# Kernel tuning notes

Measured on AMD Instinct MI355X. Metric: run time of the kernel, lower is better.

The kernel has to match this reference:

```python
import jax, jax.numpy as jnp
import numpy as np

B, T, D = 4, 2048, 2048
H, DK, DV = 16, 128, 128


def setup_inputs() -> dict:
    key = jax.random.key(0)
    ks = jax.random.split(key, 8)
    s = 1.0 / np.sqrt(D)
    return {
        "q": jax.random.normal(ks[0], (B, T, D), jnp.float32),
        "k": jax.random.normal(ks[1], (B, T, D), jnp.float32),
        "v": jax.random.normal(ks[2], (B, T, D), jnp.float32),
        "mask": jnp.tril(jnp.ones((T, T), dtype=bool)),  # True = attend
        # weights stored as [in, out] (torch Linear applies x @ W.T)
        "Wq": jax.random.normal(ks[3], (D, H * DK), jnp.float32) * s,
        "Wk": jax.random.normal(ks[4], (D, H * DK), jnp.float32) * s,
        "Wv": jax.random.normal(ks[5], (D, H * DV), jnp.float32) * s,
        "Wo": jax.random.normal(ks[6], (H * DV, D), jnp.float32) * s,
    }


def _attention(q, k, v, mask, Wq, Wk, Wv, Wo):
    # project and split heads: [B,T,H*dh] -> [B,H,T,dh]
    def split_heads(x, dh):
        b, t, _ = x.shape
        return x.reshape(b, t, H, dh).transpose(0, 2, 1, 3)

    q_i = split_heads(q @ Wq, DK)
    k_i = split_heads(k @ Wk, DK)
    v_i = split_heads(v @ Wv, DV)

    scores = jnp.einsum("bhik,bhjk->bhij", q_i, k_i) / jnp.sqrt(
        jnp.asarray(DK, q_i.dtype)
    )
    neg = -jnp.finfo(scores.dtype).max
    scores = jnp.where(mask[None, None, :, :], scores, neg)
    attn = jax.nn.softmax(scores, axis=-1)
    vals = jnp.einsum("bhij,bhjv->bhiv", attn, v_i)  # [B,H,T,dv]
    merged = vals.transpose(0, 2, 1, 3).reshape(q.shape[0], q.shape[1], H * DV)
    return merged @ Wo


def reference(q, k, v, mask, Wq, Wk, Wv, Wo):
    return _attention(q, k, v, mask, Wq, Wk, Wv, Wo)
```

## Files before the change

kernel.cpp:

```cpp
#include <hip/hip_runtime.h>
#include <hip/hip_bf16.h>

typedef __attribute__((ext_vector_type(8))) short bf16x8;
typedef __attribute__((ext_vector_type(4))) unsigned short u16x4;
typedef __attribute__((ext_vector_type(4))) float f32x4;

constexpr int Bb = 4, Tt = 2048, Dd = 2048, Hh = 16, DHd = 128;

static __device__ __forceinline__ unsigned short f2bf(float f) {
  union { float f; unsigned u; } x; x.f = f;
  unsigned r = x.u + 0x7fffu + ((x.u >> 16) & 1u);
  return (unsigned short)(r >> 16);
}

static __device__ __forceinline__ void gld16(const void* g, void* l) {
  __builtin_amdgcn_global_load_lds(
      (__attribute__((address_space(1))) void*)g,
      (__attribute__((address_space(3))) void*)l, 16, 0, 0);
}

__global__ __launch_bounds__(256) void cvt_bf16(const float* __restrict__ s,
                                                unsigned short* __restrict__ d) {
  const size_t i = ((size_t)blockIdx.x * 256 + threadIdx.x) * 8;
  float4 a = *(const float4*)(s + i);
  float4 b = *(const float4*)(s + i + 4);
  bf16x8 pk;
  pk[0] = (short)f2bf(a.x); pk[1] = (short)f2bf(a.y);
  pk[2] = (short)f2bf(a.z); pk[3] = (short)f2bf(a.w);
  pk[4] = (short)f2bf(b.x); pk[5] = (short)f2bf(b.y);
  pk[6] = (short)f2bf(b.z); pk[7] = (short)f2bf(b.w);
  *(bf16x8*)(d + i) = pk;
}

__global__ __launch_bounds__(256) void wtrans_all(
    const float* __restrict__ Wq, const float* __restrict__ Wk,
    const float* __restrict__ Wv, const float* __restrict__ Wo,
    unsigned short* __restrict__ WqT, unsigned short* __restrict__ WkT,
    unsigned short* __restrict__ WvT, unsigned short* __restrict__ WoT,
    float qscale) {
  __shared__ __align__(16) unsigned short tile[64][72];
  const float* src;
  unsigned short* dst;
  float sc = 1.0f;
  switch (blockIdx.z) {
    case 0: src = Wq; dst = WqT; sc = qscale; break;
    case 1: src = Wk; dst = WkT; break;
    case 2: src = Wv; dst = WvT; break;
    default: src = Wo; dst = WoT; break;
  }
  const int t = threadIdx.x;
  const int k0 = blockIdx.x * 64, n0 = blockIdx.y * 64;
  const int c = t & 15, r = t >> 4;
#pragma unroll
  for (int p = 0; p < 4; ++p) {
    const int rr = r + 16 * p;
    float4 v = *(const float4*)(src + (size_t)(k0 + rr) * Dd + n0 + c * 4);
    u16x4 pk;
    pk[0] = f2bf(v.x * sc); pk[1] = f2bf(v.y * sc);
    pk[2] = f2bf(v.z * sc); pk[3] = f2bf(v.w * sc);
    *(u16x4*)&tile[rr][c * 4] = pk;
  }
  __syncthreads();
#pragma unroll
  for (int p = 0; p < 4; ++p) {
    const int nn = r + 16 * p;
    u16x4 pk;
    pk[0] = tile[c * 4 + 0][nn]; pk[1] = tile[c * 4 + 1][nn];
    pk[2] = tile[c * 4 + 2][nn]; pk[3] = tile[c * 4 + 3][nn];
    *(u16x4*)(dst + (size_t)(n0 + nn) * Dd + k0 + c * 4) = pk;
  }
}

template <int OMODE>
__global__ __launch_bounds__(512, 2) void gemm256(
    const unsigned short* __restrict__ A, const unsigned short* __restrict__ Bt,
    void* __restrict__ Outp) {
  __shared__ __align__(16) unsigned short As[4 * 8192];
  __shared__ __align__(16) unsigned short Bs[4 * 8192];
  const int t = threadIdx.x, lane = t & 63, w = t >> 6;
  const int wm = w >> 2, wn = w & 3;
  const int fr = lane & 15, fq = lane >> 4;
  const int slot = blockIdx.x;
  const int orig = (slot & 7) * 32 + (slot >> 3);
  const int m0 = (orig >> 3) * 256, n0 = (orig & 7) * 256;

  f32x4 acc[8][4] = {};
  const int aoff = (wm * 128 + fr) * 32 + fq * 8;
  const int boff = (wn * 64 + fr) * 32 + fq * 8;

  auto STAGE = [&](int kt) {
    const int b = kt & 3;
    const int k0 = kt * 32;
#pragma unroll
    for (int p = 0; p < 2; ++p) {
      const int idx = t + p * 512, row = idx >> 2, ch = idx & 3;
      gld16(A + (size_t)(m0 + row) * Dd + k0 + ch * 8, &As[b * 8192 + idx * 8]);
    }
#pragma unroll
    for (int p = 0; p < 2; ++p) {
      const int idx = t + p * 512, row = idx >> 2, ch = idx & 3;
      gld16(Bt + (size_t)(n0 + row) * Dd + k0 + ch * 8, &Bs[b * 8192 + idx * 8]);
    }
  };

  constexpr int NT = Dd / 32;
  STAGE(0); STAGE(1); STAGE(2);

  for (int kt = 0; kt < NT; ++kt) {
    if (kt + 3 < NT) {
      STAGE(kt + 3);
      asm volatile("s_waitcnt vmcnt(12)" ::: "memory");
    } else if (kt + 2 < NT) {
      asm volatile("s_waitcnt vmcnt(8)" ::: "memory");
    } else if (kt + 1 < NT) {
      asm volatile("s_waitcnt vmcnt(4)" ::: "memory");
    } else {
      asm volatile("s_waitcnt vmcnt(0)" ::: "memory");
    }
    __builtin_amdgcn_sched_barrier(0);
    __builtin_amdgcn_s_barrier();
    __builtin_amdgcn_sched_barrier(0);

    const int bo = (kt & 3) * 8192;
    bf16x8 af[8], bf[4];
#pragma unroll
    for (int m = 0; m < 8; ++m)
      af[m] = *(const bf16x8*)&As[bo + aoff + m * 512];
#pragma unroll
    for (int n = 0; n < 4; ++n)
      bf[n] = *(const bf16x8*)&Bs[bo + boff + n * 512];

    __builtin_amdgcn_s_setprio(1);
#pragma unroll
    for (int m = 0; m < 8; ++m)
#pragma unroll
      for (int n = 0; n < 4; ++n)
        acc[m][n] = __builtin_amdgcn_mfma_f32_16x16x32_bf16(af[m], bf[n],
                                                            acc[m][n], 0, 0, 0);
    __builtin_amdgcn_s_setprio(0);
    __builtin_amdgcn_sched_barrier(0);
    __builtin_amdgcn_s_barrier();
  }

#pragma unroll
  for (int m = 0; m < 8; ++m) {
    const int mg = m0 + wm * 128 + m * 16 + fq * 4;
    const int bb = mg >> 11, tt0 = mg & (Tt - 1);
#pragma unroll
    for (int n = 0; n < 4; ++n) {
      const int ng = n0 + wn * 64 + n * 16 + fr;
      if (OMODE == 0) {
        float* o = (float*)Outp + (size_t)mg * Dd + ng;
#pragma unroll
        for (int r = 0; r < 4; ++r) o[(size_t)r * Dd] = acc[m][n][r];
      } else if (OMODE == 1) {
        const int h = ng >> 7, dh = ng & 127;
        unsigned short* o = (unsigned short*)Outp +
                            (((size_t)bb * Hh + h) * Tt + tt0) * DHd + dh;
#pragma unroll
        for (int r = 0; r < 4; ++r) o[r * DHd] = f2bf(acc[m][n][r]);
      } else {
        const int h = ng >> 7, dh = ng & 127;
        u16x4 pk;
#pragma unroll
        for (int r = 0; r < 4; ++r) pk[r] = f2bf(acc[m][n][r]);
        *(u16x4*)((unsigned short*)Outp +
                  (((size_t)bb * Hh + h) * DHd + dh) * Tt + tt0) = pk;
      }
    }
  }
}

__global__ __launch_bounds__(256, 2) void fattn(
    const unsigned short* __restrict__ Qp, const unsigned short* __restrict__ Kp,
    const unsigned short* __restrict__ Vt, unsigned short* __restrict__ Ao) {
  __shared__ __align__(16) unsigned short Ks[2][64 * 128];
  __shared__ __align__(16) unsigned short Vs[2][128 * 64];
  const int t = threadIdx.x, lane = t & 63, w = t >> 6;
  const int fr = lane & 15, fq = lane >> 4;
  const int rsw = fr & 7;
  const int id = blockIdx.x;
  const int xcd = id & 7, slot = id >> 3;
  const int bh = xcd * 8 + (slot >> 4);
  const int qb = 15 - (slot & 15);
  const int q0w = qb * 128 + w * 32;
  const unsigned short* Qb = Qp + (size_t)bh * Tt * DHd;
  const unsigned short* Kb = Kp + (size_t)bh * Tt * DHd;
  const unsigned short* Vb = Vt + (size_t)bh * DHd * Tt;

  bf16x8 qf[2][4];
#pragma unroll
  for (int mg = 0; mg < 2; ++mg)
#pragma unroll
    for (int ks = 0; ks < 4; ++ks)
      qf[mg][ks] = *(const bf16x8*)(Qb + (size_t)(q0w + mg * 16 + fr) * DHd +
                                    ks * 32 + fq * 8);

  f32x4 oacc[2][8] = {};
  float m_[2] = {-1e30f, -1e30f};
  float l_[2] = {0.f, 0.f};

  auto STAGE = [&](int b, int kv0) {
#pragma unroll
    for (int p = 0; p < 4; ++p) {
      const int idx = t + p * 256, row = idx >> 4, ch = idx & 15;
      gld16(Kb + (size_t)(kv0 + row) * DHd + ((ch ^ (row & 7)) * 8),
            &Ks[b][idx * 8]);
    }
#pragma unroll
    for (int p = 0; p < 4; ++p) {
      const int idx = t + p * 256, row = idx >> 3, ch = idx & 7;
      gld16(Vb + (size_t)row * Tt + kv0 + ((ch ^ (row & 7)) * 8),
            &Vs[b][idx * 8]);
    }
  };

  const int ntile = 2 * qb + 2;
  STAGE(0, 0);
  int cur = 0;

  for (int kt = 0; kt < ntile; ++kt) {
    const int kv0 = kt * 64;
    __builtin_amdgcn_s_barrier();
    if (kt + 1 < ntile) {
      STAGE(cur ^ 1, (kt + 1) * 64);
      asm volatile("s_waitcnt vmcnt(8)" ::: "memory");
    } else {
      asm volatile("s_waitcnt vmcnt(0)" ::: "memory");
    }
    __builtin_amdgcn_sched_barrier(0);
    __builtin_amdgcn_s_barrier();

    if (kv0 <= q0w + 31) {
      const unsigned short* Kc = &Ks[cur][0];
      const unsigned short* Vc = &Vs[cur][0];

      f32x4 s[2][4] = {};
      __builtin_amdgcn_s_setprio(1);
#pragma unroll
      for (int tt = 0; tt < 4; ++tt) {
        bf16x8 kf[4];
#pragma unroll
        for (int ks = 0; ks < 4; ++ks)
          kf[ks] = *(const bf16x8*)(Kc + (tt * 16 + fr) * 128 +
                                    ((ks * 4 + fq) ^ rsw) * 8);
#pragma unroll
        for (int ks = 0; ks < 4; ++ks) {
          s[0][tt] = __builtin_amdgcn_mfma_f32_16x16x32_bf16(kf[ks], qf[0][ks],
                                                             s[0][tt], 0, 0, 0);
          s[1][tt] = __builtin_amdgcn_mfma_f32_16x16x32_bf16(kf[ks], qf[1][ks],
                                                             s[1][tt], 0, 0, 0);
        }
      }
      __builtin_amdgcn_s_setprio(0);

      uint2 c[2][4];
#pragma unroll
      for (int mg = 0; mg < 2; ++mg) {
        const int qg = q0w + mg * 16;
        if (kv0 + 63 > qg) {
          const int qa = qg + fr;
#pragma unroll
          for (int tt = 0; tt < 4; ++tt)
#pragma unroll
            for (int r = 0; r < 4; ++r)
              if (kv0 + tt * 16 + fq * 4 + r > qa) s[mg][tt][r] = -1e30f;
        }

        float tmax = s[mg][0][0];
#pragma unroll
        for (int tt = 0; tt < 4; ++tt)
#pragma unroll
          for (int r = 0; r < 4; ++r) tmax = fmaxf(tmax, s[mg][tt][r]);
        tmax = fmaxf(tmax, __shfl_xor(tmax, 16));
        tmax = fmaxf(tmax, __shfl_xor(tmax, 32));

        if (!__all(tmax <= m_[mg] + 8.0f)) {
          const float mn = fmaxf(m_[mg], tmax);
          const float alpha = __builtin_amdgcn_exp2f(m_[mg] - mn);
          m_[mg] = mn;
          float al4[4];
#pragma unroll
          for (int r = 0; r < 4; ++r) al4[r] = __shfl(alpha, fq * 4 + r);
#pragma unroll
          for (int dt = 0; dt < 8; ++dt)
#pragma unroll
            for (int r = 0; r < 4; ++r) oacc[mg][dt][r] *= al4[r];
          l_[mg] *= alpha;
        }

        float rs = 0.f;
#pragma unroll
        for (int tt = 0; tt < 4; ++tt)
#pragma unroll
          for (int r = 0; r < 4; ++r) {
            const float p = __builtin_amdgcn_exp2f(s[mg][tt][r] - m_[mg]);
            s[mg][tt][r] = p;
            rs += p;
          }
        rs += __shfl_xor(rs, 16);
        rs += __shfl_xor(rs, 32);
        l_[mg] += rs;

#pragma unroll
        for (int tt = 0; tt < 4; ++tt) {
          unsigned r0, r1;
          asm("v_cvt_pk_bf16_f32 %0, %1, %2"
              : "=v"(r0) : "v"(s[mg][tt][0]), "v"(s[mg][tt][1]));
          asm("v_cvt_pk_bf16_f32 %0, %1, %2"
              : "=v"(r1) : "v"(s[mg][tt][2]), "v"(s[mg][tt][3]));
          c[mg][tt].x = r0; c[mg][tt].y = r1;
        }
      }

      const int src0 = fr + 32 * (fq & 1);
      const int src1 = src0 + 16;
      const bool hi = (fq >> 1) != 0;
      __builtin_amdgcn_s_setprio(1);
#pragma unroll
      for (int ks2 = 0; ks2 < 2; ++ks2) {
        bf16x8 pf[2];
#pragma unroll
        for (int mg = 0; mg < 2; ++mg) {
          const int a0 = __shfl((int)c[mg][2 * ks2].x, src0);
          const int b0 = __shfl((int)c[mg][2 * ks2 + 1].x, src0);
          const int a1 = __shfl((int)c[mg][2 * ks2].y, src0);
          const int b1 = __shfl((int)c[mg][2 * ks2 + 1].y, src0);
          const int a2 = __shfl((int)c[mg][2 * ks2].x, src1);
          const int b2 = __shfl((int)c[mg][2 * ks2 + 1].x, src1);
          const int a3 = __shfl((int)c[mg][2 * ks2].y, src1);
          const int b3 = __shfl((int)c[mg][2 * ks2 + 1].y, src1);
          union { int wd[4]; bf16x8 v; } pu;
          pu.wd[0] = hi ? b0 : a0;
          pu.wd[1] = hi ? b1 : a1;
          pu.wd[2] = hi ? b2 : a2;
          pu.wd[3] = hi ? b3 : a3;
          pf[mg] = pu.v;
        }
#pragma unroll
        for (int dt = 0; dt < 8; ++dt) {
          const bf16x8 vf = *(const bf16x8*)(Vc + (dt * 16 + fr) * 64 +
                                             ((ks2 * 4 + fq) ^ rsw) * 8);
          oacc[0][dt] = __builtin_amdgcn_mfma_f32_16x16x32_bf16(pf[0], vf,
                                                                oacc[0][dt], 0, 0, 0);
          oacc[1][dt] = __builtin_amdgcn_mfma_f32_16x16x32_bf16(pf[1], vf,
                                                                oacc[1][dt], 0, 0, 0);
        }
      }
      __builtin_amdgcn_s_setprio(0);
    }
    cur ^= 1;
  }

  const int bb = bh >> 4, hh = bh & 15;
#pragma unroll
  for (int mg = 0; mg < 2; ++mg) {
    float linv[4];
#pragma unroll
    for (int r = 0; r < 4; ++r) linv[r] = 1.0f / __shfl(l_[mg], fq * 4 + r);
    const int qrow = q0w + mg * 16 + fq * 4;
#pragma unroll
    for (int r = 0; r < 4; ++r) {
      unsigned short* o = Ao + ((size_t)bb * Tt + qrow + r) * Dd + hh * DHd + fr;
#pragma unroll
      for (int dt = 0; dt < 8; ++dt) o[dt * 16] = f2bf(oacc[mg][dt][r] * linv[r]);
    }
  }
}

extern "C" void kernel_launch(void* const* d_in, const int* in_sizes, int n_in,
                              void* d_out, int out_size, void* d_ws, size_t ws_size,
                              hipStream_t stream) {
  const float* q = (const float*)d_in[0];
  const float* k = (const float*)d_in[1];
  const float* v = (const float*)d_in[2];
  const float* Wq = (const float*)d_in[4];
  const float* Wk = (const float*)d_in[5];
  const float* Wv = (const float*)d_in[6];
  const float* Wo = (const float*)d_in[7];

  const size_t WE = (size_t)Dd * Dd;
  const size_t PE = (size_t)Bb * Hh * Tt * DHd;
  unsigned short* WqT = (unsigned short*)d_ws;
  unsigned short* WkT = WqT + WE;
  unsigned short* WvT = WkT + WE;
  unsigned short* WoT = WvT + WE;
  unsigned short* Qx = WoT + WE;
  unsigned short* Kx = Qx + PE;
  unsigned short* Vx = Kx + PE;
  unsigned short* Ax = Vx + PE;

  const float qscale = (float)(1.4426950408889634 / 11.313708498984761);
  wtrans_all<<<dim3(32, 32, 4), 256, 0, stream>>>(
      Wq, Wk, Wv, Wo, WqT, WkT, WvT, WoT, qscale);

  cvt_bf16<<<dim3(8192), 256, 0, stream>>>(q, Ax);
  gemm256<1><<<dim3(256), 512, 0, stream>>>(Ax, WqT, Qx);
  cvt_bf16<<<dim3(8192), 256, 0, stream>>>(k, Ax);
  gemm256<1><<<dim3(256), 512, 0, stream>>>(Ax, WkT, Kx);
  cvt_bf16<<<dim3(8192), 256, 0, stream>>>(v, Ax);
  gemm256<2><<<dim3(256), 512, 0, stream>>>(Ax, WvT, Vx);
  fattn<<<dim3(1024), 256, 0, stream>>>(Qx, Kx, Vx, Ax);
  gemm256<0><<<dim3(256), 512, 0, stream>>>(Ax, WoT, (float*)d_out);
}
```

Before: 584.0 us.

## Restructure projection GEMM into 8-phase ping-pong pipeline with swizzled LDS

Replaces the 4-stage K=32 GEMM pipeline with a double-buffered K=64 schedule. Each iteration is split into four MFMA quadrants, and the global-to-LDS loads for the next tiles are interleaved between them under barriers. LDS tiles use an XOR swizzle on 16-byte chunks so fragment reads avoid bank conflicts. The aim is to overlap memory traffic with matrix math more finely and to cut LDS conflicts, at the cost of more barriers and more complex wait-count bookkeeping.

```diff
diff --git a/kernel.cpp b/kernel.cpp
--- a/kernel.cpp
+++ b/kernel.cpp
@@ -72,71 +72,141 @@
 }
 
 template <int OMODE>
-__global__ __launch_bounds__(512, 2) void gemm256(
+__global__ __launch_bounds__(512, 2) void gemm8p(
     const unsigned short* __restrict__ A, const unsigned short* __restrict__ Bt,
     void* __restrict__ Outp) {
-  __shared__ __align__(16) unsigned short As[4 * 8192];
-  __shared__ __align__(16) unsigned short Bs[4 * 8192];
+  __shared__ __align__(16) unsigned short As[2][2][128 * 64];
+  __shared__ __align__(16) unsigned short Bs[2][2][128 * 64];
   const int t = threadIdx.x, lane = t & 63, w = t >> 6;
   const int wm = w >> 2, wn = w & 3;
   const int fr = lane & 15, fq = lane >> 4;
+  const int sw = fr & 7;
   const int slot = blockIdx.x;
   const int orig = (slot & 7) * 32 + (slot >> 3);
   const int m0 = (orig >> 3) * 256, n0 = (orig & 7) * 256;
 
+  const int srow = t >> 3, sch = t & 7;
+  const int scol = (sch ^ (srow & 7)) * 8;
+
+  auto SA = [&](int tau, int h) {
+    const unsigned short* g =
+        A + (size_t)(m0 + h * 128 + srow) * Dd + tau * 64 + scol;
+    unsigned short* l = &As[tau & 1][h][(srow * 8 + sch) * 8];
+    gld16(g, l);
+    gld16(g + (size_t)64 * Dd, l + 4096);
+  };
+  auto SB = [&](int tau, int h) {
+    const unsigned short* g =
+        Bt + (size_t)(n0 + h * 128 + srow) * Dd + tau * 64 + scol;
+    unsigned short* l = &Bs[tau & 1][h][(srow * 8 + sch) * 8];
+    gld16(g, l);
+    gld16(g + (size_t)64 * Dd, l + 4096);
+  };
+
   f32x4 acc[8][4] = {};
-  const int aoff = (wm * 128 + fr) * 32 + fq * 8;
-  const int boff = (wn * 64 + fr) * 32 + fq * 8;
-
-  auto STAGE = [&](int kt) {
-    const int b = kt & 3;
-    const int k0 = kt * 32;
-#pragma unroll
-    for (int p = 0; p < 2; ++p) {
-      const int idx = t + p * 512, row = idx >> 2, ch = idx & 3;
-      gld16(A + (size_t)(m0 + row) * Dd + k0 + ch * 8, &As[b * 8192 + idx * 8]);
-    }
-#pragma unroll
-    for (int p = 0; p < 2; ++p) {
-      const int idx = t + p * 512, row = idx >> 2, ch = idx & 3;
-      gld16(Bt + (size_t)(n0 + row) * Dd + k0 + ch * 8, &Bs[b * 8192 + idx * 8]);
-    }
-  };
-
-  constexpr int NT = Dd / 32;
-  STAGE(0); STAGE(1); STAGE(2);
-
-  for (int kt = 0; kt < NT; ++kt) {
-    if (kt + 3 < NT) {
-      STAGE(kt + 3);
-      asm volatile("s_waitcnt vmcnt(12)" ::: "memory");
-    } else if (kt + 2 < NT) {
-      asm volatile("s_waitcnt vmcnt(8)" ::: "memory");
-    } else if (kt + 1 < NT) {
+  constexpr int NT = Dd / 64;
+
+  SA(0, 0); SA(0, 1); SB(0, 0); SB(0, 1); SB(1, 0); SB(1, 1);
+  asm volatile("s_waitcnt vmcnt(4)" ::: "memory");
+  __builtin_amdgcn_s_barrier();
+  __builtin_amdgcn_sched_barrier(0);
+
+  for (int tau = 0; tau < NT; ++tau) {
+    const unsigned short* Ab = &As[tau & 1][wm][0];
+    const unsigned short* Bb = &Bs[tau & 1][wn >> 1][0];
+    const int brow = (wn & 1) * 64;
+
+    bf16x8 a0[4][2], a1[4][2], b0[2][2], b1[2][2];
+
+#pragma unroll
+    for (int i = 0; i < 4; ++i)
+#pragma unroll
+      for (int ks = 0; ks < 2; ++ks)
+        a0[i][ks] = *(const bf16x8*)&Ab[(i * 16 + fr) * 64 +
+                                        (((ks * 4 + fq) ^ sw)) * 8];
+#pragma unroll
+    for (int j = 0; j < 2; ++j)
+#pragma unroll
+      for (int ks = 0; ks < 2; ++ks)
+        b0[j][ks] = *(const bf16x8*)&Bb[(brow + j * 16 + fr) * 64 +
+                                        (((ks * 4 + fq) ^ sw)) * 8];
+    if (tau + 1 < NT) SA(tau + 1, 0);
+    __builtin_amdgcn_s_barrier();
+    __builtin_amdgcn_sched_barrier(0);
+    __builtin_amdgcn_s_setprio(1);
+#pragma unroll
+    for (int i = 0; i < 4; ++i)
+#pragma unroll
+      for (int j = 0; j < 2; ++j)
+#pragma unroll
+        for (int ks = 0; ks < 2; ++ks)
+          acc[i][j] = __builtin_amdgcn_mfma_f32_16x16x32_bf16(
+              a0[i][ks], b0[j][ks], acc[i][j], 0, 0, 0);
+    __builtin_amdgcn_s_setprio(0);
+    __builtin_amdgcn_sched_barrier(0);
+    __builtin_amdgcn_s_barrier();
+
+#pragma unroll
+    for (int j = 0; j < 2; ++j)
+#pragma unroll
+      for (int ks = 0; ks < 2; ++ks)
+        b1[j][ks] = *(const bf16x8*)&Bb[(brow + (j + 2) * 16 + fr) * 64 +
+                                        (((ks * 4 + fq) ^ sw)) * 8];
+    if (tau + 1 < NT) SA(tau + 1, 1);
+    __builtin_amdgcn_s_barrier();
+    __builtin_amdgcn_sched_barrier(0);
+    __builtin_amdgcn_s_setprio(1);
+#pragma unroll
+    for (int i = 0; i < 4; ++i)
+#pragma unroll
+      for (int j = 0; j < 2; ++j)
+#pragma unroll
+        for (int ks = 0; ks < 2; ++ks)
+          acc[i][j + 2] = __builtin_amdgcn_mfma_f32_16x16x32_bf16(
+              a0[i][ks], b1[j][ks], acc[i][j + 2], 0, 0, 0);
+    __builtin_amdgcn_s_setprio(0);
+    __builtin_amdgcn_sched_barrier(0);
+    __builtin_amdgcn_s_barrier();
+
+#pragma unroll
+    for (int i = 0; i < 4; ++i)
+#pragma unroll
+      for (int ks = 0; ks < 2; ++ks)
+        a1[i][ks] = *(const bf16x8*)&Ab[((i + 4) * 16 + fr) * 64 +
+                                        (((ks * 4 + fq) ^ sw)) * 8];
+    if (tau + 2 < NT) SB(tau + 2, 0);
+    __builtin_amdgcn_s_barrier();
+    __builtin_amdgcn_sched_barrier(0);
+    __builtin_amdgcn_s_setprio(1);
+#pragma unroll
+    for (int i = 0; i < 4; ++i)
+#pragma unroll
+      for (int j = 0; j < 2; ++j)
+#pragma unroll
+        for (int ks = 0; ks < 2; ++ks)
+          acc[i + 4][j] = __builtin_amdgcn_mfma_f32_16x16x32_bf16(
+              a1[i][ks], b0[j][ks], acc[i + 4][j], 0, 0, 0);
+    __builtin_amdgcn_s_setprio(0);
+    __builtin_amdgcn_sched_barrier(0);
+    __builtin_amdgcn_s_barrier();
+
+    if (tau + 2 < NT) {
+      SB(tau + 2, 1);
       asm volatile("s_waitcnt vmcnt(4)" ::: "memory");
-    } else {
+    } else if (tau + 1 < NT) {
       asm volatile("s_waitcnt vmcnt(0)" ::: "memory");
     }
-    __builtin_amdgcn_sched_barrier(0);
-    __builtin_amdgcn_s_barrier();
-    __builtin_amdgcn_sched_barrier(0);
-
-    const int bo = (kt & 3) * 8192;
-    bf16x8 af[8], bf[4];
-#pragma unroll
-    for (int m = 0; m < 8; ++m)
-      af[m] = *(const bf16x8*)&As[bo + aoff + m * 512];
-#pragma unroll
-    for (int n = 0; n < 4; ++n)
-      bf[n] = *(const bf16x8*)&Bs[bo + boff + n * 512];
-
+    __builtin_amdgcn_s_barrier();
+    __builtin_amdgcn_sched_barrier(0);
     __builtin_amdgcn_s_setprio(1);
 #pragma unroll
-    for (int m = 0; m < 8; ++m)
-#pragma unroll
-      for (int n = 0; n < 4; ++n)
-        acc[m][n] = __builtin_amdgcn_mfma_f32_16x16x32_bf16(af[m], bf[n],
-                                                            acc[m][n], 0, 0, 0);
+    for (int i = 0; i < 4; ++i)
+#pragma unroll
+      for (int j = 0; j < 2; ++j)
+#pragma unroll
+        for (int ks = 0; ks < 2; ++ks)
+          acc[i + 4][j + 2] = __builtin_amdgcn_mfma_f32_16x16x32_bf16(
+              a1[i][ks], b1[j][ks], acc[i + 4][j + 2], 0, 0, 0);
     __builtin_amdgcn_s_setprio(0);
     __builtin_amdgcn_sched_barrier(0);
     __builtin_amdgcn_s_barrier();
@@ -395,11 +465,11 @@
       Wq, Wk, Wv, Wo, WqT, WkT, WvT, WoT, qscale);
 
   cvt_bf16<<<dim3(8192), 256, 0, stream>>>(q, Ax);
-  gemm256<1><<<dim3(256), 512, 0, stream>>>(Ax, WqT, Qx);
+  gemm8p<1><<<dim3(256), 512, 0, stream>>>(Ax, WqT, Qx);
   cvt_bf16<<<dim3(8192), 256, 0, stream>>>(k, Ax);
-  gemm256<1><<<dim3(256), 512, 0, stream>>>(Ax, WkT, Kx);
+  gemm8p<1><<<dim3(256), 512, 0, stream>>>(Ax, WkT, Kx);
   cvt_bf16<<<dim3(8192), 256, 0, stream>>>(v, Ax);
-  gemm256<2><<<dim3(256), 512, 0, stream>>>(Ax, WvT, Vx);
+  gemm8p<2><<<dim3(256), 512, 0, stream>>>(Ax, WvT, Vx);
   fattn<<<dim3(1024), 256, 0, stream>>>(Qx, Kx, Vx, Ax);
-  gemm256<0><<<dim3(256), 512, 0, stream>>>(Ax, WoT, (float*)d_out);
-}
+  gemm8p<0><<<dim3(256), 512, 0, stream>>>(Ax, WoT, (float*)d_out);
+}
```

After: 532.2 us. 8.9% less time.
